# Kernel optimization log

Measured on AMD Instinct MI355X. Metric: run time of the kernel, lower is better.

The kernel has to match this reference:

```python
import jax, jax.numpy as jnp
import numpy as np

B, N, N_IN, N_OUT, NUM_ACTS = 65536, 512, 64, 16, 5


def setup_inputs() -> dict:
    key = jax.random.key(0)
    k1, k2, k3, k4 = jax.random.split(key, 4)
    input_values = jax.random.normal(k1, (B, N_IN), dtype=jnp.float32)
    # small weights so recurrent pre-activations stay in a sane range
    weight_matrix = jax.random.normal(k2, (N, N), dtype=jnp.float32) * 0.1
    biases = jax.random.normal(k3, (N,), dtype=jnp.float32) * 0.1
    act_ids = jax.random.randint(k4, (N,), 0, NUM_ACTS, dtype=jnp.int32)
    return {
        "input_values": input_values,
        "weight_matrix": weight_matrix,
        "biases": biases,
        "act_ids": act_ids,
    }


def _apply_lut_activations(total, act_ids):
    # Vectorized replacement for the per-neuron Python dispatch loop.
    # act_ids: [N] int, total: [B, N] float. Elementwise select fuses cleanly.
    conds = [act_ids[None, :] == k for k in range(NUM_ACTS)]
    branches = [
        jnp.tanh(total),                      # 0: tanh
        jax.nn.sigmoid(total),                # 1: sigmoid
        jax.nn.relu(total),                   # 2: relu
        jnp.where(total > 0, total, 0.01 * total),  # 3: leaky_relu
        total,                                # 4: identity
    ]
    return jnp.select(conds, branches, total)


def reference(input_values, weight_matrix, biases, act_ids):
    b, n_in = input_values.shape
    n = weight_matrix.shape[0]
    # forward_batch: states start at zeros (refractory multiply on zeros is a no-op),
    # input neurons (first N_IN indices) get the raw input values.
    states = jnp.zeros((b, n), dtype=input_values.dtype).at[:, :n_in].set(input_values)
    total_input = states @ weight_matrix + biases  # [B, N]
    activated = _apply_lut_activations(total_input, act_ids)
    # input-layer neurons keep their raw input values (loop skips layer == 'input')
    is_input = jnp.arange(n) < n_in  # [N]
    new_states = jnp.where(is_input[None, :], states, activated)
    # output neurons are the last N_OUT indices
    return new_states[:, n - N_OUT:]
```

## Files before the change

### kernel.cpp

```cpp
#include <hip/hip_runtime.h>
#include <math.h>


typedef __bf16 bf16x8 __attribute__((ext_vector_type(8)));
typedef float floatx4 __attribute__((ext_vector_type(4)));

#define NN_N 512
#define NN_NIN 64
#define NN_NOUT 16

__global__ __launch_bounds__(256) void NeuralNetwork_74466142978489_kernel(
    const float* __restrict__ x,
    const float* __restrict__ W,
    const float* __restrict__ bias,
    const int*   __restrict__ acts,
    float* __restrict__ out,
    int num_tiles)
{
    const int lane = threadIdx.x & 63;
    const int wave = (int)((blockIdx.x * blockDim.x + threadIdx.x) >> 6);
    const int nwaves = (int)((gridDim.x * blockDim.x) >> 6);
    const int m    = lane & 15;
    const int quad = lane >> 4;
    const int col  = m;
    const int gcol = NN_N - NN_NOUT + col;

    bf16x8 bfrag0, bfrag1;
#pragma unroll
    for (int j = 0; j < 8; ++j) {
        int k0 = quad * 8 + j;
        bfrag0[j] = (__bf16)W[(size_t)k0 * NN_N + gcol];
        bfrag1[j] = (__bf16)W[(size_t)(k0 + 32) * NN_N + gcol];
    }
    const float bval = bias[gcol];
    const int aid = acts[gcol];

    for (int tile = wave; tile < num_tiles; tile += nwaves) {
        const float* row = x + (size_t)(tile * 16 + m) * NN_NIN;

        floatx4 acc = {bval, bval, bval, bval};
#pragma unroll
        for (int t = 0; t < 2; ++t) {
            const float4 a0 = *(const float4*)(row + t * 32 + quad * 8);
            const float4 a1 = *(const float4*)(row + t * 32 + quad * 8 + 4);
            bf16x8 afrag;
            afrag[0] = (__bf16)a0.x; afrag[1] = (__bf16)a0.y;
            afrag[2] = (__bf16)a0.z; afrag[3] = (__bf16)a0.w;
            afrag[4] = (__bf16)a1.x; afrag[5] = (__bf16)a1.y;
            afrag[6] = (__bf16)a1.z; afrag[7] = (__bf16)a1.w;
            acc = __builtin_amdgcn_mfma_f32_16x16x32_bf16(
                afrag, (t == 0) ? bfrag0 : bfrag1, acc, 0, 0, 0);
        }

#pragma unroll
        for (int r = 0; r < 4; ++r) {
            float v = acc[r];
            float y;
            if (aid == 0) {
                y = 1.0f - 2.0f / (__expf(2.0f * v) + 1.0f);
            } else if (aid == 1) {
                y = 1.0f / (1.0f + __expf(-v));
            } else if (aid == 2) {
                y = v > 0.0f ? v : 0.0f;
            } else if (aid == 3) {
                y = v > 0.0f ? v : 0.01f * v;
            } else {
                y = v;
            }
            out[(size_t)(tile * 16 + quad * 4 + r) * NN_NOUT + col] = y;
        }
    }
}

extern "C" void kernel_launch(void* const* d_in, const int* in_sizes, int n_in,
                              void* d_out, int out_size, void* d_ws, size_t ws_size,
                              hipStream_t stream) {
    const float* x    = (const float*)d_in[0];
    const float* W    = (const float*)d_in[1];
    const float* bias = (const float*)d_in[2];
    const int*   acts = (const int*)d_in[3];
    float* out = (float*)d_out;

    const int B = in_sizes[0] / NN_NIN;
    const int num_tiles = B / 16;

    const int block = 256;
    const int waves_per_block = block / 64;
    const int grid = (num_tiles + waves_per_block - 1) / waves_per_block;

    NeuralNetwork_74466142978489_kernel<<<grid, block, 0, stream>>>(
        x, W, bias, acts, out, num_tiles);
}
```

Baseline: 70.91 us.

## Process two tiles per wave with hoisted nontemporal input loads

Each wave now handles two 16-row tiles. All input loads for both tiles are issued up front, before the weight fragment loads, and use nontemporal loads, with nontemporal stores for the outputs. The grid shrinks by half to match. The aim is more memory-level parallelism per wave and amortising the per-wave W/bias fragment loads, at the cost of more registers and fewer waves to hide latency.

```diff
diff --git a/kernel.cpp b/kernel.cpp
--- a/kernel.cpp
+++ b/kernel.cpp
@@ -8,6 +8,7 @@
 #define NN_N 512
 #define NN_NIN 64
 #define NN_NOUT 16
+#define TPW 2
 
 __global__ __launch_bounds__(256) void NeuralNetwork_74466142978489_kernel(
     const float* __restrict__ x,
@@ -19,55 +20,74 @@
 {
     const int lane = threadIdx.x & 63;
     const int wave = (int)((blockIdx.x * blockDim.x + threadIdx.x) >> 6);
-    const int nwaves = (int)((gridDim.x * blockDim.x) >> 6);
     const int m    = lane & 15;
     const int quad = lane >> 4;
-    const int col  = m;
-    const int gcol = NN_N - NN_NOUT + col;
+    const int gcol = NN_N - NN_NOUT + m;
+
+    const int tile0 = wave * TPW;
+    if (tile0 >= num_tiles) return;
+    const int ntile = (num_tiles - tile0 < TPW) ? (num_tiles - tile0) : TPW;
+
+    floatx4 a[TPW][4];
+#pragma unroll
+    for (int u = 0; u < TPW; ++u) {
+        if (u < ntile) {
+            const float* row = x + (size_t)((tile0 + u) * 16 + m) * NN_NIN;
+#pragma unroll
+            for (int t = 0; t < 2; ++t) {
+                a[u][2 * t] = __builtin_nontemporal_load(
+                    reinterpret_cast<const floatx4*>(row + t * 32 + quad * 8));
+                a[u][2 * t + 1] = __builtin_nontemporal_load(
+                    reinterpret_cast<const floatx4*>(row + t * 32 + quad * 8 + 4));
+            }
+        }
+    }
 
     bf16x8 bfrag0, bfrag1;
 #pragma unroll
     for (int j = 0; j < 8; ++j) {
-        int k0 = quad * 8 + j;
-        bfrag0[j] = (__bf16)W[(size_t)k0 * NN_N + gcol];
-        bfrag1[j] = (__bf16)W[(size_t)(k0 + 32) * NN_N + gcol];
+        const int k0 = quad * 8 + j;
+        bfrag0[j] = (__bf16)W[k0 * NN_N + gcol];
+        bfrag1[j] = (__bf16)W[(k0 + 32) * NN_N + gcol];
     }
     const float bval = bias[gcol];
     const int aid = acts[gcol];
 
-    for (int tile = wave; tile < num_tiles; tile += nwaves) {
-        const float* row = x + (size_t)(tile * 16 + m) * NN_NIN;
+#pragma unroll
+    for (int u = 0; u < TPW; ++u) {
+        if (u < ntile) {
+            floatx4 acc = {bval, bval, bval, bval};
+#pragma unroll
+            for (int t = 0; t < 2; ++t) {
+                bf16x8 af;
+#pragma unroll
+                for (int e = 0; e < 4; ++e) {
+                    af[e]     = (__bf16)a[u][2 * t][e];
+                    af[e + 4] = (__bf16)a[u][2 * t + 1][e];
+                }
+                acc = __builtin_amdgcn_mfma_f32_16x16x32_bf16(
+                    af, (t == 0) ? bfrag0 : bfrag1, acc, 0, 0, 0);
+            }
 
-        floatx4 acc = {bval, bval, bval, bval};
+            const int rowbase = (tile0 + u) * 16 + quad * 4;
 #pragma unroll
-        for (int t = 0; t < 2; ++t) {
-            const float4 a0 = *(const float4*)(row + t * 32 + quad * 8);
-            const float4 a1 = *(const float4*)(row + t * 32 + quad * 8 + 4);
-            bf16x8 afrag;
-            afrag[0] = (__bf16)a0.x; afrag[1] = (__bf16)a0.y;
-            afrag[2] = (__bf16)a0.z; afrag[3] = (__bf16)a0.w;
-            afrag[4] = (__bf16)a1.x; afrag[5] = (__bf16)a1.y;
-            afrag[6] = (__bf16)a1.z; afrag[7] = (__bf16)a1.w;
-            acc = __builtin_amdgcn_mfma_f32_16x16x32_bf16(
-                afrag, (t == 0) ? bfrag0 : bfrag1, acc, 0, 0, 0);
-        }
-
-#pragma unroll
-        for (int r = 0; r < 4; ++r) {
-            float v = acc[r];
-            float y;
-            if (aid == 0) {
-                y = 1.0f - 2.0f / (__expf(2.0f * v) + 1.0f);
-            } else if (aid == 1) {
-                y = 1.0f / (1.0f + __expf(-v));
-            } else if (aid == 2) {
-                y = v > 0.0f ? v : 0.0f;
-            } else if (aid == 3) {
-                y = v > 0.0f ? v : 0.01f * v;
-            } else {
-                y = v;
+            for (int r = 0; r < 4; ++r) {
+                float v = acc[r];
+                float y;
+                if (aid == 0) {
+                    y = 1.0f - 2.0f / (__expf(2.0f * v) + 1.0f);
+                } else if (aid == 1) {
+                    y = 1.0f / (1.0f + __expf(-v));
+                } else if (aid == 2) {
+                    y = v > 0.0f ? v : 0.0f;
+                } else if (aid == 3) {
+                    y = v > 0.0f ? v : 0.01f * v;
+                } else {
+                    y = v;
+                }
+                __builtin_nontemporal_store(
+                    y, out + (size_t)(rowbase + r) * NN_NOUT + m);
             }
-            out[(size_t)(tile * 16 + quad * 4 + r) * NN_NOUT + col] = y;
         }
     }
 }
@@ -86,7 +106,8 @@
 
     const int block = 256;
     const int waves_per_block = block / 64;
-    const int grid = (num_tiles + waves_per_block - 1) / waves_per_block;
+    const int waves = (num_tiles + TPW - 1) / TPW;
+    const int grid = (waves + waves_per_block - 1) / waves_per_block;
 
     NeuralNetwork_74466142978489_kernel<<<grid, block, 0, stream>>>(
         x, W, bias, acts, out, num_tiles);
```

After: 72.01 us. No clear change (+1.5%).
